# Kernel tuning notes

Measured on AMD Instinct MI355X. Metric: run time of the kernel, lower is better.

## Reference

```python
import jax, jax.numpy as jnp
import numpy as np

HIDDEN_DIM = 256
N = 8192


def setup_inputs() -> dict:
    key = jax.random.key(0)
    k1, k2, k3, k4 = jax.random.split(key, 4)
    img = jax.random.normal(k1, (N, HIDDEN_DIM), dtype=jnp.float32)
    text = jax.random.normal(k2, (N, HIDDEN_DIM), dtype=jnp.float32)
    # nn.Linear(hidden_dim, hidden_dim, bias=False) weights, shape [out, in]
    scale = 1.0 / np.sqrt(HIDDEN_DIM)
    Wq = jax.random.uniform(k3, (HIDDEN_DIM, HIDDEN_DIM), dtype=jnp.float32, minval=-scale, maxval=scale)
    Wk = jax.random.uniform(k4, (HIDDEN_DIM, HIDDEN_DIM), dtype=jnp.float32, minval=-scale, maxval=scale)
    return {"img": img, "text": text, "Wq": Wq, "Wk": Wk}


def reference(img, text, Wq, Wk):
    d = img.shape[-1]
    norm_fact = 1.0 / jnp.sqrt(jnp.asarray(d, dtype=img.dtype))
    Q = img @ Wq.T                       # [N, D]
    K = text @ Wk.T                      # [N, D]
    scores = Q @ K.T                     # [N, N]
    # softmax over dim=1 (keys), then scaled by 1/sqrt(D)
    attn = jax.nn.softmax(scores, axis=1) * norm_fact
    out_img = attn @ img                 # [N, D]
    out_text = attn @ text               # [N, D]
    return (out_img, out_text)
```

## Files before the change

### kernel.cpp

```cpp
#include <hip/hip_runtime.h>

typedef unsigned short ushort_t;
typedef unsigned int uint_t;
typedef __attribute__((ext_vector_type(8))) short short8;
typedef __attribute__((ext_vector_type(8))) _Float16 half8;
typedef __attribute__((ext_vector_type(4))) _Float16 half4;
typedef __attribute__((ext_vector_type(4))) float float4v;

#define MFMA_BF16(a, b, c) __builtin_amdgcn_mfma_f32_16x16x32_bf16((a), (b), (c), 0, 0, 0)
#define MFMA_F16(a, b, c) __builtin_amdgcn_mfma_f32_16x16x32_f16((a), (b), (c), 0, 0, 0)

#define NQ 8192
#define DIM 256
#define DV 512

__device__ __forceinline__ ushort_t f2bf(float x) {
  union { float f; uint_t u; } v; v.f = x;
  return (ushort_t)((v.u + 0x7fffu + ((v.u >> 16) & 1u)) >> 16);
}
__device__ __forceinline__ float bf2f(ushort_t b) {
  union { uint_t u; float f; } v; v.u = ((uint_t)b) << 16;
  return v.f;
}

__device__ __forceinline__ half8 cvt8h(const float* p) {
  float4v a = *(const float4v*)p;
  float4v b = *(const float4v*)(p + 4);
  half8 r;
  r[0] = (_Float16)a[0]; r[1] = (_Float16)a[1];
  r[2] = (_Float16)a[2]; r[3] = (_Float16)a[3];
  r[4] = (_Float16)b[0]; r[5] = (_Float16)b[1];
  r[6] = (_Float16)b[2]; r[7] = (_Float16)b[3];
  return r;
}

__device__ __forceinline__ half8 as_h8(short8 s) {
  union { short8 s; half8 h; } u; u.s = s; return u.h;
}

__device__ __forceinline__ void load_lds_16(const void* g, void* l) {
  __builtin_amdgcn_global_load_lds(
      (const __attribute__((address_space(1))) uint_t*)g,
      (__attribute__((address_space(3))) uint_t*)l, 16, 0, 0);
}

__global__ __launch_bounds__(256, 2) void proj_kernel(
    const float* __restrict__ img, const float* __restrict__ text,
    const float* __restrict__ Wq, const float* __restrict__ Wk,
    _Float16* __restrict__ Qh, _Float16* __restrict__ Kh) {
  const int lane = threadIdx.x & 63;
  const int wv = threadIdx.x >> 6;
  const int l16 = lane & 15;
  const int quad = lane >> 4;
  const float* A = blockIdx.z ? text : img;
  const float* W = blockIdx.z ? Wk : Wq;
  _Float16* C = blockIdx.z ? Kh : Qh;
  const int row = blockIdx.x * 64 + wv * 16 + l16;
  const int colbase = blockIdx.y * 64;

  float4v acc[4];
#pragma unroll
  for (int c = 0; c < 4; ++c) acc[c] = (float4v){0.f, 0.f, 0.f, 0.f};

#pragma unroll
  for (int f = 0; f < 8; ++f) {
    const int k0 = f * 32 + quad * 8;
    half8 af = cvt8h(A + (size_t)row * DIM + k0);
#pragma unroll
    for (int c = 0; c < 4; ++c) {
      half8 bfr = cvt8h(W + (size_t)(colbase + c * 16 + l16) * DIM + k0);
      acc[c] = MFMA_F16(af, bfr, acc[c]);
    }
  }
  const int rbase = blockIdx.x * 64 + wv * 16 + quad * 4;
#pragma unroll
  for (int c = 0; c < 4; ++c)
#pragma unroll
    for (int r = 0; r < 4; ++r)
      C[(size_t)(rbase + r) * DIM + colbase + c * 16 + l16] = (_Float16)acc[c][r];
}

__global__ __launch_bounds__(256) void make_vt_kernel(
    const float* __restrict__ img, const float* __restrict__ text,
    ushort_t* __restrict__ Vt) {
  __shared__ float tile[64][65];
  const int n0 = blockIdx.x * 64;
  const int c0 = blockIdx.y * 64;
  const float* src = (c0 < 256) ? img : text;
  const int cc0 = (c0 < 256) ? c0 : (c0 - 256);
  const int tid = threadIdx.x;

#pragma unroll
  for (int i = 0; i < 4; ++i) {
    const int r = i * 16 + (tid >> 4);
    const int c = (tid & 15) * 4;
    *(float4v*)&tile[r][c] = *(const float4v*)(src + (size_t)(n0 + r) * DIM + cc0 + c);
  }
  __syncthreads();
  const int c = tid >> 2;
  const int seg = tid & 3;
  ushort_t tmp[16];
#pragma unroll
  for (int t = 0; t < 16; ++t) tmp[t] = f2bf(tile[seg * 16 + t][c]);
  ushort_t* dst = Vt + (size_t)(c0 + c) * NQ + n0 + seg * 16;
  *(short8*)dst = *(short8*)&tmp[0];
  *(short8*)(dst + 8) = *(short8*)&tmp[8];
}

__global__ __launch_bounds__(256, 2) void attn_kernel(
    const _Float16* __restrict__ Qh, const _Float16* __restrict__ Kh,
    const ushort_t* __restrict__ Vt, _Float16* __restrict__ pacc,
    float* __restrict__ pdenom, int kps, int ks) {
  __shared__ __align__(16) ushort_t ldsK[32 * DIM];
  __shared__ __align__(16) ushort_t ldsV[DV * 32];
  __shared__ __align__(16) ushort_t ldsP[64 * 32];

  const int tid = threadIdx.x;
  const int lane = tid & 63;
  const int wv = tid >> 6;
  const int l16 = lane & 15;
  const int quad = lane >> 4;
  const int id = blockIdx.x;
  int qtile, split;
  if (ks == 8) {
    split = id & 7;
    qtile = id >> 3;
  } else if (ks == 4) {
    split = (id & 7) >> 1;
    qtile = ((id >> 3) << 1) | (id & 1);
  } else {
    split = id >> 7;
    qtile = id & 127;
  }
  const int kbeg = split * kps;
  const int sw2 = (l16 >> 1) & 3;

  short8 qf[8];
  {
    const _Float16* qptr = Qh + (size_t)(qtile * 64 + wv * 16 + l16) * DIM;
#pragma unroll
    for (int f = 0; f < 8; ++f)
      qf[f] = *(const short8*)(qptr + f * 32 + quad * 8);
  }

  float4v acc[4][8];
#pragma unroll
  for (int m = 0; m < 4; ++m)
#pragma unroll
    for (int c = 0; c < 8; ++c) acc[m][c] = (float4v){0.f, 0.f, 0.f, 0.f};
  float dacc[4] = {0.f, 0.f, 0.f, 0.f};

  const int ntiles = kps >> 5;
  for (int it = 0; it < ntiles; ++it) {
    const int k0 = kbeg + it * 32;
    __syncthreads();
#pragma unroll
    for (int i = 0; i < 4; ++i) {
      const int chunk = i * 256 + tid;
      const int n = chunk >> 5;
      const int cs = (chunk & 31) ^ (n & 7);
      load_lds_16(Kh + (size_t)(k0 + n) * DIM + cs * 8,
                  (char*)ldsK + (i * 256 + wv * 64) * 16);
    }
#pragma unroll
    for (int i = 0; i < 8; ++i) {
      const int chunk = i * 256 + tid;
      const int vrow = chunk >> 2;
      const int dc = (chunk & 3) ^ ((vrow >> 1) & 3);
      load_lds_16(Vt + (size_t)vrow * NQ + k0 + dc * 8,
                  (char*)ldsV + (i * 256 + wv * 64) * 16);
    }
    __syncthreads();

    float4v s0 = (float4v){0.f, 0.f, 0.f, 0.f};
    float4v s1 = (float4v){0.f, 0.f, 0.f, 0.f};
    const int swk = l16 & 7;
#pragma unroll
    for (int f = 0; f < 8; ++f) {
      const int cs = ((f * 4 + quad) ^ swk) * 8;
      short8 kb0 = *(const short8*)(ldsK + l16 * DIM + cs);
      short8 kb1 = *(const short8*)(ldsK + (l16 + 16) * DIM + cs);
      s0 = MFMA_F16(as_h8(qf[f]), as_h8(kb0), s0);
      s1 = MFMA_F16(as_h8(qf[f]), as_h8(kb1), s1);
    }

    ushort_t pb0[4], pb1[4];
#pragma unroll
    for (int r = 0; r < 4; ++r) {
      pb0[r] = f2bf(__expf(s0[r]));
      pb1[r] = f2bf(__expf(s1[r]));
    }
#pragma unroll
    for (int r = 0; r < 4; ++r) {
      float t = bf2f(pb0[r]) + bf2f(pb1[r]);
      t += __shfl_xor(t, 1);
      t += __shfl_xor(t, 2);
      t += __shfl_xor(t, 4);
      t += __shfl_xor(t, 8);
      dacc[r] += t;
    }
#pragma unroll
    for (int r = 0; r < 4; ++r) {
      const int rb = wv * 16 + quad * 4 + r;
      const int swp = (rb >> 1) & 3;
      ldsP[rb * 32 + ((l16 >> 3) ^ swp) * 8 + (l16 & 7)] = pb0[r];
      ldsP[rb * 32 + ((2 + (l16 >> 3)) ^ swp) * 8 + (l16 & 7)] = pb1[r];
    }
    __syncthreads();

    short8 pa[4];
#pragma unroll
    for (int m = 0; m < 4; ++m)
      pa[m] = *(const short8*)(ldsP + (m * 16 + l16) * 32 + (quad ^ sw2) * 8);
#pragma unroll
    for (int c = 0; c < 8; ++c) {
      const int vcol = (wv * 8 + c) * 16 + l16;
      short8 vb = *(const short8*)(ldsV + vcol * 32 + (quad ^ sw2) * 8);
#pragma unroll
      for (int m = 0; m < 4; ++m)
        acc[m][c] = MFMA_BF16(pa[m], vb, acc[m][c]);
    }
  }

  __syncthreads();
  float* ldsD = (float*)ldsP;
  if (l16 == 0) {
#pragma unroll
    for (int r = 0; r < 4; ++r)
      ldsD[wv * 16 + quad * 4 + r] = dacc[r];
  }
  __syncthreads();

  _Float16* pout = pacc + (size_t)split * ((size_t)NQ * DV);
#pragma unroll
  for (int m = 0; m < 4; ++m) {
    float invd[4];
#pragma unroll
    for (int r = 0; r < 4; ++r) invd[r] = 1.0f / ldsD[m * 16 + quad * 4 + r];
    const int rowbase = qtile * 64 + m * 16 + quad * 4;
#pragma unroll
    for (int c = 0; c < 8; ++c) {
      const int col = (wv * 8 + c) * 16 + l16;
#pragma unroll
      for (int r = 0; r < 4; ++r)
        pout[(size_t)(rowbase + r) * DV + col] = (_Float16)(acc[m][c][r] * invd[r]);
    }
  }
  if (l16 == 0) {
    const int rowbase = qtile * 64 + wv * 16 + quad * 4;
#pragma unroll
    for (int r = 0; r < 4; ++r)
      pdenom[split * NQ + rowbase + r] = dacc[r];
  }
}

__global__ __launch_bounds__(256) void combine_kernel(
    const _Float16* __restrict__ pacc, const float* __restrict__ pdenom,
    float* __restrict__ out, int ks) {
  const int idx = blockIdx.x * 256 + threadIdx.x;
  const int n = idx >> 7;
  const int c4 = (idx & 127) << 2;
  float4v s = (float4v){0.f, 0.f, 0.f, 0.f};
  float dsum = 0.f;
  for (int sp = 0; sp < ks; ++sp) {
    const float d = pdenom[sp * NQ + n];
    half4 x = *(const half4*)(pacc + (size_t)sp * ((size_t)NQ * DV) + (size_t)n * DV + c4);
    s[0] += d * (float)x[0];
    s[1] += d * (float)x[1];
    s[2] += d * (float)x[2];
    s[3] += d * (float)x[3];
    dsum += d;
  }
  const float scale = 1.0f / (16.0f * dsum);
  s *= scale;
  float* dst = (c4 < 256) ? (out + (size_t)n * DIM + c4)
                          : (out + (size_t)NQ * DIM + (size_t)n * DIM + (c4 - 256));
  *(float4v*)dst = s;
}

extern "C" void kernel_launch(void* const* d_in, const int* in_sizes, int n_in,
                              void* d_out, int out_size, void* d_ws, size_t ws_size,
                              hipStream_t stream) {
  const float* img = (const float*)d_in[0];
  const float* text = (const float*)d_in[1];
  const float* Wq = (const float*)d_in[2];
  const float* Wk = (const float*)d_in[3];
  float* out = (float*)d_out;
  char* ws = (char*)d_ws;

  _Float16* Qh = (_Float16*)ws;
  _Float16* Kh = (_Float16*)(ws + ((size_t)4 << 20));
  ushort_t* Vt = (ushort_t*)(ws + ((size_t)8 << 20));
  const size_t accsz = (size_t)NQ * DV * sizeof(_Float16);
  const size_t base = (size_t)16 << 20;

  int ks = 8;
  if (ws_size < base + 8 * (accsz + NQ * sizeof(float))) ks = 4;
  if (ws_size < base + 4 * (accsz + NQ * sizeof(float))) ks = 2;
  _Float16* pacc = (_Float16*)(ws + base);
  float* pdenom = (float*)(ws + base + (size_t)ks * accsz);

  hipLaunchKernelGGL(proj_kernel, dim3(128, 4, 2), dim3(256), 0, stream,
                     img, text, Wq, Wk, Qh, Kh);
  hipLaunchKernelGGL(make_vt_kernel, dim3(128, 8), dim3(256), 0, stream,
                     img, text, Vt);
  hipLaunchKernelGGL(attn_kernel, dim3(128 * ks), dim3(256), 0, stream,
                     Qh, Kh, Vt, pacc, pdenom, NQ / ks, ks);
  hipLaunchKernelGGL(combine_kernel, dim3((NQ * DV / 4) / 256), dim3(256), 0, stream,
                     pacc, pdenom, out, ks);
}
```

Baseline: 280.6 us.

## Double-buffer K/V tiles in LDS and enlarge attention query tile to 128 rows

```diff
diff --git a/kernel.cpp b/kernel.cpp
--- a/kernel.cpp
+++ b/kernel.cpp
@@ -42,6 +42,13 @@
   __builtin_amdgcn_global_load_lds(
       (const __attribute__((address_space(1))) uint_t*)g,
       (__attribute__((address_space(3))) uint_t*)l, 16, 0, 0);
+}
+
+__device__ __forceinline__ void barrier_vm0() {
+  asm volatile("s_waitcnt vmcnt(0)\ns_barrier" ::: "memory");
+}
+__device__ __forceinline__ void barrier_lgkm0() {
+  asm volatile("s_waitcnt lgkmcnt(0)\ns_barrier" ::: "memory");
 }
 
 __global__ __launch_bounds__(256, 2) void proj_kernel(
@@ -107,13 +114,12 @@
   *(short8*)(dst + 8) = *(short8*)&tmp[8];
 }
 
-__global__ __launch_bounds__(256, 2) void attn_kernel(
+__global__ __launch_bounds__(256, 1) void attn_kernel(
     const _Float16* __restrict__ Qh, const _Float16* __restrict__ Kh,
     const ushort_t* __restrict__ Vt, _Float16* __restrict__ pacc,
     float* __restrict__ pdenom, int kps, int ks) {
-  __shared__ __align__(16) ushort_t ldsK[32 * DIM];
-  __shared__ __align__(16) ushort_t ldsV[DV * 32];
-  __shared__ __align__(16) ushort_t ldsP[64 * 32];
+  extern __shared__ __align__(16) ushort_t smem[];
+  ushort_t* ldsP = smem + 49152;
 
   const int tid = threadIdx.x;
   const int lane = tid & 63;
@@ -121,46 +127,40 @@
   const int l16 = lane & 15;
   const int quad = lane >> 4;
   const int id = blockIdx.x;
-  int qtile, split;
-  if (ks == 8) {
-    split = id & 7;
-    qtile = id >> 3;
-  } else if (ks == 4) {
-    split = (id & 7) >> 1;
-    qtile = ((id >> 3) << 1) | (id & 1);
-  } else {
-    split = id >> 7;
-    qtile = id & 127;
-  }
+  const int split = id & (ks - 1);
+  const int qtile = id / ks;
   const int kbeg = split * kps;
   const int sw2 = (l16 >> 1) & 3;
-
-  short8 qf[8];
+  const int swk = l16 & 7;
+
+  short8 qf[2][8];
+#pragma unroll
+  for (int mm = 0; mm < 2; ++mm) {
+    const _Float16* qptr =
+        Qh + (size_t)(qtile * 128 + wv * 32 + mm * 16 + l16) * DIM;
+#pragma unroll
+    for (int f = 0; f < 8; ++f)
+      qf[mm][f] = *(const short8*)(qptr + f * 32 + quad * 8);
+  }
+
+  float4v acc[8][8];
+#pragma unroll
+  for (int m = 0; m < 8; ++m)
+#pragma unroll
+    for (int c = 0; c < 8; ++c) acc[m][c] = (float4v){0.f, 0.f, 0.f, 0.f};
+  float dacc[2][4] = {{0.f, 0.f, 0.f, 0.f}, {0.f, 0.f, 0.f, 0.f}};
+
+  const int ntiles = kps >> 5;
+
   {
-    const _Float16* qptr = Qh + (size_t)(qtile * 64 + wv * 16 + l16) * DIM;
-#pragma unroll
-    for (int f = 0; f < 8; ++f)
-      qf[f] = *(const short8*)(qptr + f * 32 + quad * 8);
-  }
-
-  float4v acc[4][8];
-#pragma unroll
-  for (int m = 0; m < 4; ++m)
-#pragma unroll
-    for (int c = 0; c < 8; ++c) acc[m][c] = (float4v){0.f, 0.f, 0.f, 0.f};
-  float dacc[4] = {0.f, 0.f, 0.f, 0.f};
-
-  const int ntiles = kps >> 5;
-  for (int it = 0; it < ntiles; ++it) {
-    const int k0 = kbeg + it * 32;
-    __syncthreads();
+    const int k0 = kbeg;
 #pragma unroll
     for (int i = 0; i < 4; ++i) {
       const int chunk = i * 256 + tid;
       const int n = chunk >> 5;
       const int cs = (chunk & 31) ^ (n & 7);
       load_lds_16(Kh + (size_t)(k0 + n) * DIM + cs * 8,
-                  (char*)ldsK + (i * 256 + wv * 64) * 16);
+                  (char*)smem + (i * 256 + wv * 64) * 16);
     }
 #pragma unroll
     for (int i = 0; i < 8; ++i) {
@@ -168,76 +168,107 @@
       const int vrow = chunk >> 2;
       const int dc = (chunk & 3) ^ ((vrow >> 1) & 3);
       load_lds_16(Vt + (size_t)vrow * NQ + k0 + dc * 8,
-                  (char*)ldsV + (i * 256 + wv * 64) * 16);
-    }
-    __syncthreads();
-
-    float4v s0 = (float4v){0.f, 0.f, 0.f, 0.f};
-    float4v s1 = (float4v){0.f, 0.f, 0.f, 0.f};
-    const int swk = l16 & 7;
+                  (char*)(smem + 16384) + (i * 256 + wv * 64) * 16);
+    }
+  }
+
+  for (int t = 0; t < ntiles; ++t) {
+    const int b = t & 1;
+    ushort_t* Kt = smem + b * 8192;
+    ushort_t* Vtile = smem + 16384 + b * 16384;
+    barrier_vm0();
+    if (t + 1 < ntiles) {
+      const int k0 = kbeg + (t + 1) * 32;
+      const int nb = (t + 1) & 1;
+      ushort_t* Kn = smem + nb * 8192;
+      ushort_t* Vn = smem + 16384 + nb * 16384;
+#pragma unroll
+      for (int i = 0; i < 4; ++i) {
+        const int chunk = i * 256 + tid;
+        const int n = chunk >> 5;
+        const int cs = (chunk & 31) ^ (n & 7);
+        load_lds_16(Kh + (size_t)(k0 + n) * DIM + cs * 8,
+                    (char*)Kn + (i * 256 + wv * 64) * 16);
+      }
+#pragma unroll
+      for (int i = 0; i < 8; ++i) {
+        const int chunk = i * 256 + tid;
+        const int vrow = chunk >> 2;
+        const int dc = (chunk & 3) ^ ((vrow >> 1) & 3);
+        load_lds_16(Vt + (size_t)vrow * NQ + k0 + dc * 8,
+                    (char*)Vn + (i * 256 + wv * 64) * 16);
+      }
+    }
+
+    float4v s00 = (float4v){0.f, 0.f, 0.f, 0.f};
+    float4v s01 = (float4v){0.f, 0.f, 0.f, 0.f};
+    float4v s10 = (float4v){0.f, 0.f, 0.f, 0.f};
+    float4v s11 = (float4v){0.f, 0.f, 0.f, 0.f};
 #pragma unroll
     for (int f = 0; f < 8; ++f) {
       const int cs = ((f * 4 + quad) ^ swk) * 8;
-      short8 kb0 = *(const short8*)(ldsK + l16 * DIM + cs);
-      short8 kb1 = *(const short8*)(ldsK + (l16 + 16) * DIM + cs);
-      s0 = MFMA_F16(as_h8(qf[f]), as_h8(kb0), s0);
-      s1 = MFMA_F16(as_h8(qf[f]), as_h8(kb1), s1);
-    }
-
-    ushort_t pb0[4], pb1[4];
-#pragma unroll
-    for (int r = 0; r < 4; ++r) {
-      pb0[r] = f2bf(__expf(s0[r]));
-      pb1[r] = f2bf(__expf(s1[r]));
-    }
-#pragma unroll
-    for (int r = 0; r < 4; ++r) {
-      float t = bf2f(pb0[r]) + bf2f(pb1[r]);
-      t += __shfl_xor(t, 1);
-      t += __shfl_xor(t, 2);
-      t += __shfl_xor(t, 4);
-      t += __shfl_xor(t, 8);
-      dacc[r] += t;
-    }
-#pragma unroll
-    for (int r = 0; r < 4; ++r) {
-      const int rb = wv * 16 + quad * 4 + r;
-      const int swp = (rb >> 1) & 3;
-      ldsP[rb * 32 + ((l16 >> 3) ^ swp) * 8 + (l16 & 7)] = pb0[r];
-      ldsP[rb * 32 + ((2 + (l16 >> 3)) ^ swp) * 8 + (l16 & 7)] = pb1[r];
-    }
-    __syncthreads();
-
-    short8 pa[4];
-#pragma unroll
-    for (int m = 0; m < 4; ++m)
+      short8 kb0 = *(const short8*)(Kt + l16 * DIM + cs);
+      short8 kb1 = *(const short8*)(Kt + (l16 + 16) * DIM + cs);
+      s00 = MFMA_F16(as_h8(qf[0][f]), as_h8(kb0), s00);
+      s01 = MFMA_F16(as_h8(qf[0][f]), as_h8(kb1), s01);
+      s10 = MFMA_F16(as_h8(qf[1][f]), as_h8(kb0), s10);
+      s11 = MFMA_F16(as_h8(qf[1][f]), as_h8(kb1), s11);
+    }
+
+#pragma unroll
+    for (int mm = 0; mm < 2; ++mm) {
+      const float4v sa = mm ? s10 : s00;
+      const float4v sb = mm ? s11 : s01;
+#pragma unroll
+      for (int r = 0; r < 4; ++r) {
+        const ushort_t p0 = f2bf(__expf(sa[r]));
+        const ushort_t p1 = f2bf(__expf(sb[r]));
+        float tsum = bf2f(p0) + bf2f(p1);
+        tsum += __shfl_xor(tsum, 1);
+        tsum += __shfl_xor(tsum, 2);
+        tsum += __shfl_xor(tsum, 4);
+        tsum += __shfl_xor(tsum, 8);
+        dacc[mm][r] += tsum;
+        const int rb = wv * 32 + mm * 16 + quad * 4 + r;
+        const int swp = (rb >> 1) & 3;
+        ldsP[rb * 32 + ((l16 >> 3) ^ swp) * 8 + (l16 & 7)] = p0;
+        ldsP[rb * 32 + ((2 + (l16 >> 3)) ^ swp) * 8 + (l16 & 7)] = p1;
+      }
+    }
+    barrier_lgkm0();
+
+    short8 pa[8];
+#pragma unroll
+    for (int m = 0; m < 8; ++m)
       pa[m] = *(const short8*)(ldsP + (m * 16 + l16) * 32 + (quad ^ sw2) * 8);
 #pragma unroll
     for (int c = 0; c < 8; ++c) {
       const int vcol = (wv * 8 + c) * 16 + l16;
-      short8 vb = *(const short8*)(ldsV + vcol * 32 + (quad ^ sw2) * 8);
-#pragma unroll
-      for (int m = 0; m < 4; ++m)
+      short8 vb = *(const short8*)(Vtile + vcol * 32 + (quad ^ sw2) * 8);
+#pragma unroll
+      for (int m = 0; m < 8; ++m)
         acc[m][c] = MFMA_BF16(pa[m], vb, acc[m][c]);
     }
   }
 
-  __syncthreads();
+  asm volatile("s_barrier" ::: "memory");
   float* ldsD = (float*)ldsP;
   if (l16 == 0) {
 #pragma unroll
-    for (int r = 0; r < 4; ++r)
-      ldsD[wv * 16 + quad * 4 + r] = dacc[r];
-  }
-  __syncthreads();
+    for (int mm = 0; mm < 2; ++mm)
+#pragma unroll
+      for (int r = 0; r < 4; ++r)
+        ldsD[wv * 32 + mm * 16 + quad * 4 + r] = dacc[mm][r];
+  }
+  barrier_lgkm0();
 
   _Float16* pout = pacc + (size_t)split * ((size_t)NQ * DV);
 #pragma unroll
-  for (int m = 0; m < 4; ++m) {
+  for (int m = 0; m < 8; ++m) {
     float invd[4];
 #pragma unroll
     for (int r = 0; r < 4; ++r) invd[r] = 1.0f / ldsD[m * 16 + quad * 4 + r];
-    const int rowbase = qtile * 64 + m * 16 + quad * 4;
+    const int rowbase = qtile * 128 + m * 16 + quad * 4;
 #pragma unroll
     for (int c = 0; c < 8; ++c) {
       const int col = (wv * 8 + c) * 16 + l16;
@@ -247,10 +278,12 @@
     }
   }
   if (l16 == 0) {
-    const int rowbase = qtile * 64 + wv * 16 + quad * 4;
-#pragma unroll
-    for (int r = 0; r < 4; ++r)
-      pdenom[split * NQ + rowbase + r] = dacc[r];
+#pragma unroll
+    for (int mm = 0; mm < 2; ++mm)
+#pragma unroll
+      for (int r = 0; r < 4; ++r)
+        pdenom[split * NQ + qtile * 128 + wv * 32 + mm * 16 + quad * 4 + r] =
+            dacc[mm][r];
   }
 }
 
@@ -294,8 +327,7 @@
   const size_t accsz = (size_t)NQ * DV * sizeof(_Float16);
   const size_t base = (size_t)16 << 20;
 
-  int ks = 8;
-  if (ws_size < base + 8 * (accsz + NQ * sizeof(float))) ks = 4;
+  int ks = 4;
   if (ws_size < base + 4 * (accsz + NQ * sizeof(float))) ks = 2;
   _Float16* pacc = (_Float16*)(ws + base);
   float* pdenom = (float*)(ws + base + (size_t)ks * accsz);
@@ -304,7 +336,8 @@
                      img, text, Wq, Wk, Qh, Kh);
   hipLaunchKernelGGL(make_vt_kernel, dim3(128, 8), dim3(256), 0, stream,
                      img, text, Vt);
-  hipLaunchKernelGGL(attn_kernel, dim3(128 * ks), dim3(256), 0, stream,
+  hipLaunchKernelGGL(attn_kernel, dim3(64 * ks), dim3(256),
+                     53248 * sizeof(ushort_t), stream,
                      Qh, Kh, Vt, pacc, pdenom, NQ / ks, ks);
   hipLaunchKernelGGL(combine_kernel, dim3((NQ * DV / 4) / 256), dim3(256), 0, stream,
                      pacc, pdenom, out, ks);
```

Measured after the change: 291.1 us. +3.7%, slower.

## Software-pipeline attention K/V/P staging and merge projection and transpose kernels

Applied to the files above, without the earlier changes.

```diff
diff --git a/kernel.cpp b/kernel.cpp
--- a/kernel.cpp
+++ b/kernel.cpp
@@ -44,76 +44,107 @@
       (__attribute__((address_space(3))) uint_t*)l, 16, 0, 0);
 }
 
-__global__ __launch_bounds__(256, 2) void proj_kernel(
+__device__ __forceinline__ void barrier_vm0_lgkm0() {
+  asm volatile("s_waitcnt vmcnt(0) lgkmcnt(0)\ns_barrier" ::: "memory");
+}
+__device__ __forceinline__ void barrier_lgkm0() {
+  asm volatile("s_waitcnt lgkmcnt(0)\ns_barrier" ::: "memory");
+}
+
+__global__ __launch_bounds__(256, 2) void pre_kernel(
     const float* __restrict__ img, const float* __restrict__ text,
     const float* __restrict__ Wq, const float* __restrict__ Wk,
-    _Float16* __restrict__ Qh, _Float16* __restrict__ Kh) {
-  const int lane = threadIdx.x & 63;
-  const int wv = threadIdx.x >> 6;
-  const int l16 = lane & 15;
-  const int quad = lane >> 4;
-  const float* A = blockIdx.z ? text : img;
-  const float* W = blockIdx.z ? Wk : Wq;
-  _Float16* C = blockIdx.z ? Kh : Qh;
-  const int row = blockIdx.x * 64 + wv * 16 + l16;
-  const int colbase = blockIdx.y * 64;
-
-  float4v acc[4];
-#pragma unroll
-  for (int c = 0; c < 4; ++c) acc[c] = (float4v){0.f, 0.f, 0.f, 0.f};
-
-#pragma unroll
-  for (int f = 0; f < 8; ++f) {
-    const int k0 = f * 32 + quad * 8;
-    half8 af = cvt8h(A + (size_t)row * DIM + k0);
-#pragma unroll
-    for (int c = 0; c < 4; ++c) {
-      half8 bfr = cvt8h(W + (size_t)(colbase + c * 16 + l16) * DIM + k0);
-      acc[c] = MFMA_F16(af, bfr, acc[c]);
-    }
-  }
-  const int rbase = blockIdx.x * 64 + wv * 16 + quad * 4;
-#pragma unroll
-  for (int c = 0; c < 4; ++c)
-#pragma unroll
-    for (int r = 0; r < 4; ++r)
-      C[(size_t)(rbase + r) * DIM + colbase + c * 16 + l16] = (_Float16)acc[c][r];
-}
-
-__global__ __launch_bounds__(256) void make_vt_kernel(
-    const float* __restrict__ img, const float* __restrict__ text,
+    _Float16* __restrict__ Qh, _Float16* __restrict__ Kh,
     ushort_t* __restrict__ Vt) {
   __shared__ float tile[64][65];
-  const int n0 = blockIdx.x * 64;
-  const int c0 = blockIdx.y * 64;
-  const float* src = (c0 < 256) ? img : text;
-  const int cc0 = (c0 < 256) ? c0 : (c0 - 256);
+  const int bid = blockIdx.x;
   const int tid = threadIdx.x;
-
+  if (bid < 1024) {
+    const int bx = bid & 127;
+    const int by = (bid >> 7) & 3;
+    const int bz = bid >> 9;
+    const int lane = tid & 63;
+    const int wv = tid >> 6;
+    const int l16 = lane & 15;
+    const int quad = lane >> 4;
+    const float* A = bz ? text : img;
+    const float* W = bz ? Wk : Wq;
+    _Float16* C = bz ? Kh : Qh;
+    const int row = bx * 64 + wv * 16 + l16;
+    const int colbase = by * 64;
+
+    float4v acc[4];
+#pragma unroll
+    for (int c = 0; c < 4; ++c) acc[c] = (float4v){0.f, 0.f, 0.f, 0.f};
+#pragma unroll
+    for (int f = 0; f < 8; ++f) {
+      const int k0 = f * 32 + quad * 8;
+      half8 af = cvt8h(A + (size_t)row * DIM + k0);
+#pragma unroll
+      for (int c = 0; c < 4; ++c) {
+        half8 bfr = cvt8h(W + (size_t)(colbase + c * 16 + l16) * DIM + k0);
+        acc[c] = MFMA_F16(af, bfr, acc[c]);
+      }
+    }
+    const int rbase = bx * 64 + wv * 16 + quad * 4;
+#pragma unroll
+    for (int c = 0; c < 4; ++c)
+#pragma unroll
+      for (int r = 0; r < 4; ++r)
+        C[(size_t)(rbase + r) * DIM + colbase + c * 16 + l16] = (_Float16)acc[c][r];
+  } else {
+    const int vb = bid - 1024;
+    const int n0 = (vb & 127) * 64;
+    const int c0 = (vb >> 7) * 64;
+    const float* src = (c0 < 256) ? img : text;
+    const int cc0 = (c0 < 256) ? c0 : (c0 - 256);
+#pragma unroll
+    for (int i = 0; i < 4; ++i) {
+      const int r = i * 16 + (tid >> 4);
+      const int c = (tid & 15) * 4;
+      *(float4v*)&tile[r][c] = *(const float4v*)(src + (size_t)(n0 + r) * DIM + cc0 + c);
+    }
+    __syncthreads();
+    const int c = tid >> 2;
+    const int seg = tid & 3;
+    ushort_t tmp[16];
+#pragma unroll
+    for (int t = 0; t < 16; ++t) tmp[t] = f2bf(tile[seg * 16 + t][c]);
+    ushort_t* dst = Vt + (size_t)(c0 + c) * NQ + n0 + seg * 16;
+    *(short8*)dst = *(short8*)&tmp[0];
+    *(short8*)(dst + 8) = *(short8*)&tmp[8];
+  }
+}
+
+__device__ __forceinline__ void stage_K(const _Float16* __restrict__ Kh, int k0,
+                                        ushort_t* dst, int tid, int wv) {
 #pragma unroll
   for (int i = 0; i < 4; ++i) {
-    const int r = i * 16 + (tid >> 4);
-    const int c = (tid & 15) * 4;
-    *(float4v*)&tile[r][c] = *(const float4v*)(src + (size_t)(n0 + r) * DIM + cc0 + c);
-  }
-  __syncthreads();
-  const int c = tid >> 2;
-  const int seg = tid & 3;
-  ushort_t tmp[16];
-#pragma unroll
-  for (int t = 0; t < 16; ++t) tmp[t] = f2bf(tile[seg * 16 + t][c]);
-  ushort_t* dst = Vt + (size_t)(c0 + c) * NQ + n0 + seg * 16;
-  *(short8*)dst = *(short8*)&tmp[0];
-  *(short8*)(dst + 8) = *(short8*)&tmp[8];
+    const int chunk = i * 256 + tid;
+    const int n = chunk >> 5;
+    const int cs = (chunk & 31) ^ (n & 7);
+    load_lds_16(Kh + (size_t)(k0 + n) * DIM + cs * 8,
+                (char*)dst + (i * 256 + wv * 64) * 16);
+  }
+}
+__device__ __forceinline__ void stage_V(const ushort_t* __restrict__ Vt, int k0,
+                                        ushort_t* dst, int tid, int wv) {
+#pragma unroll
+  for (int i = 0; i < 8; ++i) {
+    const int chunk = i * 256 + tid;
+    const int vrow = chunk >> 2;
+    const int dc = (chunk & 3) ^ ((vrow >> 1) & 3);
+    load_lds_16(Vt + (size_t)vrow * NQ + k0 + dc * 8,
+                (char*)dst + (i * 256 + wv * 64) * 16);
+  }
 }
 
 __global__ __launch_bounds__(256, 2) void attn_kernel(
     const _Float16* __restrict__ Qh, const _Float16* __restrict__ Kh,
     const ushort_t* __restrict__ Vt, _Float16* __restrict__ pacc,
     float* __restrict__ pdenom, int kps, int ks) {
-  __shared__ __align__(16) ushort_t ldsK[32 * DIM];
-  __shared__ __align__(16) ushort_t ldsV[DV * 32];
-  __shared__ __align__(16) ushort_t ldsP[64 * 32];
+  extern __shared__ __align__(16) ushort_t smem[];
+  ushort_t* ldsV = smem + 16384;
 
   const int tid = threadIdx.x;
   const int lane = tid & 63;
@@ -121,19 +152,11 @@
   const int l16 = lane & 15;
   const int quad = lane >> 4;
   const int id = blockIdx.x;
-  int qtile, split;
-  if (ks == 8) {
-    split = id & 7;
-    qtile = id >> 3;
-  } else if (ks == 4) {
-    split = (id & 7) >> 1;
-    qtile = ((id >> 3) << 1) | (id & 1);
-  } else {
-    split = id >> 7;
-    qtile = id & 127;
-  }
+  const int split = id & (ks - 1);
+  const int qtile = id / ks;
   const int kbeg = split * kps;
   const int sw2 = (l16 >> 1) & 3;
+  const int swk = l16 & 7;
 
   short8 qf[8];
   {
@@ -151,39 +174,47 @@
   float dacc[4] = {0.f, 0.f, 0.f, 0.f};
 
   const int ntiles = kps >> 5;
-  for (int it = 0; it < ntiles; ++it) {
-    const int k0 = kbeg + it * 32;
-    __syncthreads();
-#pragma unroll
-    for (int i = 0; i < 4; ++i) {
-      const int chunk = i * 256 + tid;
-      const int n = chunk >> 5;
-      const int cs = (chunk & 31) ^ (n & 7);
-      load_lds_16(Kh + (size_t)(k0 + n) * DIM + cs * 8,
-                  (char*)ldsK + (i * 256 + wv * 64) * 16);
-    }
-#pragma unroll
-    for (int i = 0; i < 8; ++i) {
-      const int chunk = i * 256 + tid;
-      const int vrow = chunk >> 2;
-      const int dc = (chunk & 3) ^ ((vrow >> 1) & 3);
-      load_lds_16(Vt + (size_t)vrow * NQ + k0 + dc * 8,
-                  (char*)ldsV + (i * 256 + wv * 64) * 16);
-    }
-    __syncthreads();
+
+  stage_K(Kh, kbeg, smem, tid, wv);
+  stage_V(Vt, kbeg, ldsV, tid, wv);
+
+  for (int t = 0; t < ntiles; ++t) {
+    const ushort_t* Kt = smem + (t & 1) * 8192;
+    barrier_vm0_lgkm0();
+    if (t + 1 < ntiles)
+      stage_K(Kh, kbeg + (t + 1) * 32, smem + ((t + 1) & 1) * 8192, tid, wv);
+
+    if (t > 0) {
+      const ushort_t* Pprev = smem + 32768 + ((t - 1) & 1) * 2048;
+      short8 pa[4];
+#pragma unroll
+      for (int m = 0; m < 4; ++m)
+        pa[m] = *(const short8*)(Pprev + (m * 16 + l16) * 32 + (quad ^ sw2) * 8);
+#pragma unroll
+      for (int c = 0; c < 8; ++c) {
+        const int vcol = (wv * 8 + c) * 16 + l16;
+        short8 vb = *(const short8*)(ldsV + vcol * 32 + (quad ^ sw2) * 8);
+#pragma unroll
+        for (int m = 0; m < 4; ++m)
+          acc[m][c] = MFMA_BF16(pa[m], vb, acc[m][c]);
+      }
+    }
 
     float4v s0 = (float4v){0.f, 0.f, 0.f, 0.f};
     float4v s1 = (float4v){0.f, 0.f, 0.f, 0.f};
-    const int swk = l16 & 7;
 #pragma unroll
     for (int f = 0; f < 8; ++f) {
       const int cs = ((f * 4 + quad) ^ swk) * 8;
-      short8 kb0 = *(const short8*)(ldsK + l16 * DIM + cs);
-      short8 kb1 = *(const short8*)(ldsK + (l16 + 16) * DIM + cs);
+      short8 kb0 = *(const short8*)(Kt + l16 * DIM + cs);
+      short8 kb1 = *(const short8*)(Kt + (l16 + 16) * DIM + cs);
       s0 = MFMA_F16(as_h8(qf[f]), as_h8(kb0), s0);
       s1 = MFMA_F16(as_h8(qf[f]), as_h8(kb1), s1);
     }
 
+    barrier_lgkm0();
+    if (t >= 1) stage_V(Vt, kbeg + t * 32, ldsV, tid, wv);
+
+    ushort_t* Pcur = smem + 32768 + (t & 1) * 2048;
     ushort_t pb0[4], pb1[4];
 #pragma unroll
     for (int r = 0; r < 4; ++r) {
@@ -192,26 +223,29 @@
     }
 #pragma unroll
     for (int r = 0; r < 4; ++r) {
-      float t = bf2f(pb0[r]) + bf2f(pb1[r]);
-      t += __shfl_xor(t, 1);
-      t += __shfl_xor(t, 2);
-      t += __shfl_xor(t, 4);
-      t += __shfl_xor(t, 8);
-      dacc[r] += t;
+      float ts = bf2f(pb0[r]) + bf2f(pb1[r]);
+      ts += __shfl_xor(ts, 1);
+      ts += __shfl_xor(ts, 2);
+      ts += __shfl_xor(ts, 4);
+      ts += __shfl_xor(ts, 8);
+      dacc[r] += ts;
     }
 #pragma unroll
     for (int r = 0; r < 4; ++r) {
       const int rb = wv * 16 + quad * 4 + r;
       const int swp = (rb >> 1) & 3;
-      ldsP[rb * 32 + ((l16 >> 3) ^ swp) * 8 + (l16 & 7)] = pb0[r];
-      ldsP[rb * 32 + ((2 + (l16 >> 3)) ^ swp) * 8 + (l16 & 7)] = pb1[r];
-    }
-    __syncthreads();
-
+      Pcur[rb * 32 + ((l16 >> 3) ^ swp) * 8 + (l16 & 7)] = pb0[r];
+      Pcur[rb * 32 + ((2 + (l16 >> 3)) ^ swp) * 8 + (l16 & 7)] = pb1[r];
+    }
+  }
+
+  barrier_vm0_lgkm0();
+  {
+    const ushort_t* Pprev = smem + 32768 + ((ntiles - 1) & 1) * 2048;
     short8 pa[4];
 #pragma unroll
     for (int m = 0; m < 4; ++m)
-      pa[m] = *(const short8*)(ldsP + (m * 16 + l16) * 32 + (quad ^ sw2) * 8);
+      pa[m] = *(const short8*)(Pprev + (m * 16 + l16) * 32 + (quad ^ sw2) * 8);
 #pragma unroll
     for (int c = 0; c < 8; ++c) {
       const int vcol = (wv * 8 + c) * 16 + l16;
@@ -222,14 +256,14 @@
     }
   }
 
-  __syncthreads();
-  float* ldsD = (float*)ldsP;
+  barrier_lgkm0();
+  float* ldsD = (float*)smem;
   if (l16 == 0) {
 #pragma unroll
     for (int r = 0; r < 4; ++r)
       ldsD[wv * 16 + quad * 4 + r] = dacc[r];
   }
-  __syncthreads();
+  barrier_lgkm0();
 
   _Float16* pout = pacc + (size_t)split * ((size_t)NQ * DV);
 #pragma unroll
@@ -294,17 +328,15 @@
   const size_t accsz = (size_t)NQ * DV * sizeof(_Float16);
   const size_t base = (size_t)16 << 20;
 
-  int ks = 8;
-  if (ws_size < base + 8 * (accsz + NQ * sizeof(float))) ks = 4;
+  int ks = 4;
   if (ws_size < base + 4 * (accsz + NQ * sizeof(float))) ks = 2;
   _Float16* pacc = (_Float16*)(ws + base);
   float* pdenom = (float*)(ws + base + (size_t)ks * accsz);
 
-  hipLaunchKernelGGL(proj_kernel, dim3(128, 4, 2), dim3(256), 0, stream,
-                     img, text, Wq, Wk, Qh, Kh);
-  hipLaunchKernelGGL(make_vt_kernel, dim3(128, 8), dim3(256), 0, stream,
-                     img, text, Vt);
-  hipLaunchKernelGGL(attn_kernel, dim3(128 * ks), dim3(256), 0, stream,
+  hipLaunchKernelGGL(pre_kernel, dim3(2048), dim3(256), 0, stream,
+                     img, text, Wq, Wk, Qh, Kh, Vt);
+  hipLaunchKernelGGL(attn_kernel, dim3(128 * ks), dim3(256),
+                     36864 * sizeof(ushort_t), stream,
                      Qh, Kh, Vt, pacc, pdenom, NQ / ks, ks);
   hipLaunchKernelGGL(combine_kernel, dim3((NQ * DV / 4) / 256), dim3(256), 0, stream,
                      pacc, pdenom, out, ks);
```

After: 263.3 us. 1.07x faster.
